# Optimization experiments

Hardware: AMD Instinct MI355X
Metric: run time of the kernel (lower is better)

Reference implementation:

```python
import jax, jax.numpy as jnp
import numpy as np

EPS = 1e-12  # tf.math.l2_normalize epsilon

def _l2norm(v, axis):
    # matches tf.math.l2_normalize: x * rsqrt(max(sum(x^2), eps))
    sq = jnp.sum(v * v, axis=axis, keepdims=True)
    return v * jax.lax.rsqrt(jnp.maximum(sq, EPS))

def setup_inputs() -> dict:
    key = jax.random.key(0)
    ks = jax.random.split(key, 6)
    N, H, W, D, K, OUT = 32, 32, 32, 512, 64, 4096
    x = jax.random.normal(ks[0], (N, H, W, D), dtype=jnp.float32)
    conv1_w = jax.random.normal(ks[1], (D, K), dtype=jnp.float32) * (1.0 / np.sqrt(D))
    conv1_b = jax.random.normal(ks[2], (K,), dtype=jnp.float32) * 0.01
    C = jax.random.uniform(ks[3], (D, K), dtype=jnp.float32)  # tf.random.uniform init
    conv2_w = jax.random.normal(ks[4], (K * D, OUT), dtype=jnp.float32) * (1.0 / np.sqrt(K * D))
    conv2_b = jax.random.normal(ks[5], (OUT,), dtype=jnp.float32) * 0.01
    return {"x": x, "conv1_w": conv1_w, "conv1_b": conv1_b, "C": C,
            "conv2_w": conv2_w, "conv2_b": conv2_b}

def reference(x, conv1_w, conv1_b, C, conv2_w, conv2_b):
    N = x.shape[0]
    # 1x1 conv -> soft assignment over clusters (softmax over last axis)
    s = jax.nn.softmax(jnp.einsum('nhwd,dk->nhwk', x, conv1_w) + conv1_b, axis=-1)  # [N,H,W,K]
    # VLAD: v[n,k,d] = sum_hw s[n,h,w,k] * (x[n,h,w,d] + C[d,k])
    # distributive form avoids the [N,H,W,D,K] intermediate (same math):
    v = jnp.einsum('nhwk,nhwd->nkd', s, x) + jnp.sum(s, axis=(1, 2))[:, :, None] * C.T[None]  # [N,K,D]
    # postnorm: intra-cluster L2 then global-descriptor L2
    v = _l2norm(v, axis=-1)
    v = v.reshape(N, -1)          # flatten [N, K*D]
    v = _l2norm(v, axis=-1)
    # final 1x1 conv (dense projection) + global l2_normalize (tf axis=None)
    v = v @ conv2_w + conv2_b     # [N, 4096]
    v = _l2norm(v, axis=None)     # normalize over the whole tensor (faithful to source)
    return v
```

## Files before the change

### kernel.cpp

```cpp
#include <hip/hip_runtime.h>
#include <math.h>

#define EPSF 1e-12f

typedef __attribute__((ext_vector_type(8))) short short8v;
typedef __attribute__((ext_vector_type(4))) float f32x4;

__device__ __forceinline__ unsigned short f2bf(float f) {
    unsigned int u = __float_as_uint(f);
    return (unsigned short)((u + 0x7FFF + ((u >> 16) & 1)) >> 16);
}
__device__ __forceinline__ float bf2f(unsigned short h) {
    return __uint_as_float(((unsigned int)h) << 16);
}

__global__ __launch_bounds__(256) void k_prep(
    const float* __restrict__ w1, const float* __restrict__ C,
    unsigned short* __restrict__ w1t_h, unsigned short* __restrict__ w1t_l,
    float* __restrict__ Ct)
{
    const int i  = blockIdx.x * 256 + threadIdx.x;
    const int k  = i >> 7;
    const int d0 = (i & 127) << 2;
    float vv[4], cc[4];
#pragma unroll
    for (int j = 0; j < 4; ++j) {
        vv[j] = w1[(size_t)(d0 + j) * 64 + k];
        cc[j] = C [(size_t)(d0 + j) * 64 + k];
    }
    ushort4 h, l;
    h.x = f2bf(vv[0]); l.x = f2bf(vv[0] - bf2f(h.x));
    h.y = f2bf(vv[1]); l.y = f2bf(vv[1] - bf2f(h.y));
    h.z = f2bf(vv[2]); l.z = f2bf(vv[2] - bf2f(h.z));
    h.w = f2bf(vv[3]); l.w = f2bf(vv[3] - bf2f(h.w));
    *(ushort4*)(w1t_h + (size_t)k * 512 + d0) = h;
    *(ushort4*)(w1t_l + (size_t)k * 512 + d0) = l;
    *(float4*)(Ct + (size_t)k * 512 + d0) = make_float4(cc[0], cc[1], cc[2], cc[3]);
}

__global__ __launch_bounds__(256) void k_assign(
    const float* __restrict__ x,
    const unsigned short* __restrict__ w1t_h,
    const unsigned short* __restrict__ w1t_l,
    const float* __restrict__ b1,
    unsigned short* __restrict__ st_h, unsigned short* __restrict__ st_l,
    float* __restrict__ ap)
{
    const int tid  = threadIdx.x;
    const int lane = tid & 63;
    const int wv   = __builtin_amdgcn_readfirstlane(tid >> 6);
    const int l4   = lane >> 4;
    const int l16  = lane & 15;
    const int pix0 = blockIdx.x * 64;
    const int n_img  = blockIdx.x >> 4;
    const int p_base = (blockIdx.x & 15) * 64;

    __shared__ unsigned short Xh[64][72];
    __shared__ unsigned short Xl[64][72];
    __shared__ unsigned short Wh[64][72];
    __shared__ unsigned short Wl[64][72];
    __shared__ float apred[4][64];

    f32x4 acc[4];
#pragma unroll
    for (int nf = 0; nf < 4; ++nf) acc[nf] = (f32x4){0.f, 0.f, 0.f, 0.f};

    float4  xr[4];
    short8v wrh[2], wrl[2];
#pragma unroll
    for (int t = 0; t < 4; ++t) {
        int idx = tid + t * 256, p = idx >> 4, d4 = (idx & 15) << 2;
        xr[t] = *(const float4*)&x[(size_t)(pix0 + p) * 512 + d4];
    }
#pragma unroll
    for (int q = 0; q < 2; ++q) {
        int i = (q * 256 + tid) * 8, k = i >> 6, dd = i & 63;
        wrh[q] = *(const short8v*)(w1t_h + (size_t)k * 512 + dd);
        wrl[q] = *(const short8v*)(w1t_l + (size_t)k * 512 + dd);
    }

    for (int c = 0; c < 8; ++c) {
#pragma unroll
        for (int t = 0; t < 4; ++t) {
            int idx = tid + t * 256, p = idx >> 4, d4 = (idx & 15) << 2;
            float4 v = xr[t];
            ushort4 h4, l4v;
            h4.x = f2bf(v.x); l4v.x = f2bf(v.x - bf2f(h4.x));
            h4.y = f2bf(v.y); l4v.y = f2bf(v.y - bf2f(h4.y));
            h4.z = f2bf(v.z); l4v.z = f2bf(v.z - bf2f(h4.z));
            h4.w = f2bf(v.w); l4v.w = f2bf(v.w - bf2f(h4.w));
            *(ushort4*)&Xh[p][d4] = h4;
            *(ushort4*)&Xl[p][d4] = l4v;
        }
#pragma unroll
        for (int q = 0; q < 2; ++q) {
            int i = (q * 256 + tid) * 8, k = i >> 6, dd = i & 63;
            *(short8v*)&Wh[k][dd] = wrh[q];
            *(short8v*)&Wl[k][dd] = wrl[q];
        }
        if (c + 1 < 8) {
#pragma unroll
            for (int t = 0; t < 4; ++t) {
                int idx = tid + t * 256, p = idx >> 4, d4 = (idx & 15) << 2;
                xr[t] = *(const float4*)&x[(size_t)(pix0 + p) * 512 +
                                           (c + 1) * 64 + d4];
            }
#pragma unroll
            for (int q = 0; q < 2; ++q) {
                int i = (q * 256 + tid) * 8, k = i >> 6, dd = i & 63;
                wrh[q] = *(const short8v*)(w1t_h + (size_t)k * 512 +
                                           (c + 1) * 64 + dd);
                wrl[q] = *(const short8v*)(w1t_l + (size_t)k * 512 +
                                           (c + 1) * 64 + dd);
            }
        }
        __syncthreads();
#pragma unroll
        for (int ks = 0; ks < 2; ++ks) {
            short8v ah = *(const short8v*)&Xh[wv * 16 + l16][ks * 32 + l4 * 8];
            short8v al = *(const short8v*)&Xl[wv * 16 + l16][ks * 32 + l4 * 8];
#pragma unroll
            for (int nf = 0; nf < 4; ++nf) {
                short8v bh = *(const short8v*)&Wh[nf * 16 + l16][ks * 32 + l4 * 8];
                short8v bl = *(const short8v*)&Wl[nf * 16 + l16][ks * 32 + l4 * 8];
                acc[nf] = __builtin_amdgcn_mfma_f32_16x16x32_bf16(ah, bh, acc[nf], 0, 0, 0);
                acc[nf] = __builtin_amdgcn_mfma_f32_16x16x32_bf16(ah, bl, acc[nf], 0, 0, 0);
                acc[nf] = __builtin_amdgcn_mfma_f32_16x16x32_bf16(al, bh, acc[nf], 0, 0, 0);
            }
        }
        __syncthreads();
    }

    float lg[4][4];
#pragma unroll
    for (int nf = 0; nf < 4; ++nf) {
        const float bb = b1[nf * 16 + l16];
#pragma unroll
        for (int r = 0; r < 4; ++r) lg[nf][r] = acc[nf][r] + bb;
    }
    float mx[4], sm[4];
#pragma unroll
    for (int r = 0; r < 4; ++r)
        mx[r] = fmaxf(fmaxf(lg[0][r], lg[1][r]), fmaxf(lg[2][r], lg[3][r]));
#pragma unroll
    for (int m = 1; m <= 8; m <<= 1)
#pragma unroll
        for (int r = 0; r < 4; ++r) mx[r] = fmaxf(mx[r], __shfl_xor(mx[r], m, 64));
#pragma unroll
    for (int r = 0; r < 4; ++r) sm[r] = 0.f;
#pragma unroll
    for (int nf = 0; nf < 4; ++nf)
#pragma unroll
        for (int r = 0; r < 4; ++r) { lg[nf][r] = __expf(lg[nf][r] - mx[r]); sm[r] += lg[nf][r]; }
#pragma unroll
    for (int m = 1; m <= 8; m <<= 1)
#pragma unroll
        for (int r = 0; r < 4; ++r) sm[r] += __shfl_xor(sm[r], m, 64);

#pragma unroll
    for (int nf = 0; nf < 4; ++nf) {
        float sv[4];
        ushort4 hh, ll;
#pragma unroll
        for (int r = 0; r < 4; ++r) sv[r] = lg[nf][r] * (1.0f / sm[r]);
        hh.x = f2bf(sv[0]); ll.x = f2bf(sv[0] - bf2f(hh.x));
        hh.y = f2bf(sv[1]); ll.y = f2bf(sv[1] - bf2f(hh.y));
        hh.z = f2bf(sv[2]); ll.z = f2bf(sv[2] - bf2f(hh.z));
        hh.w = f2bf(sv[3]); ll.w = f2bf(sv[3] - bf2f(hh.w));
        const size_t so = (size_t)(n_img * 64 + nf * 16 + l16) * 1024 +
                          p_base + wv * 16 + l4 * 4;
        *(ushort4*)(st_h + so) = hh;
        *(ushort4*)(st_l + so) = ll;
        float tsum = sv[0] + sv[1] + sv[2] + sv[3];
        tsum += __shfl_xor(tsum, 16, 64);
        tsum += __shfl_xor(tsum, 32, 64);
        if (l4 == 0) apred[wv][nf * 16 + l16] = tsum;
    }
    __syncthreads();
    if (tid < 64)
        ap[(size_t)blockIdx.x * 64 + tid] =
            (apred[0][tid] + apred[1][tid]) + (apred[2][tid] + apred[3][tid]);
}

__global__ __launch_bounds__(128) void k_vlad(
    const unsigned short* __restrict__ st_h,
    const unsigned short* __restrict__ st_l,
    const float* __restrict__ x, float* __restrict__ vpart)
{
    __shared__ float X2[2][32][32];

    const int tid  = threadIdx.x;
    const int lane = tid & 63;
    const int w    = __builtin_amdgcn_readfirstlane(tid >> 6);
    const int l4   = lane >> 4;
    const int l16  = lane & 15;
    const int b    = blockIdx.x;
    const int n    = b >> 5;
    const int ph   = (b >> 4) & 1;
    const int dc   = b & 15;
    const int dbase = dc * 32;
    const int pbase = n * 1024 + ph * 512;

    f32x4 acc[4];
#pragma unroll
    for (int mf = 0; mf < 4; ++mf) acc[mf] = (f32x4){0.f, 0.f, 0.f, 0.f};

#define VSTAGE(T_, B_)                                                        \
    do {                                                                      \
        _Pragma("unroll")                                                     \
        for (int i_ = 0; i_ < 2; ++i_) {                                      \
            const int jj_ = w * 2 + i_;                                       \
            __builtin_amdgcn_global_load_lds(                                 \
                (const __attribute__((address_space(1))) void*)               \
                    (x + (size_t)(pbase + (T_) * 32 + jj_ * 8 +               \
                                  (lane >> 3)) * 512 + dbase + (lane & 7) * 4), \
                (__attribute__((address_space(3))) void*)&X2[B_][jj_ * 8][0], \
                16, 0, 0);                                                    \
        }                                                                     \
    } while (0)

    VSTAGE(0, 0);
    __syncthreads();

    int buf = 0;
    for (int t = 0; t < 16; ++t) {
        if (t + 1 < 16) VSTAGE(t + 1, buf ^ 1);

        const size_t sbase = (size_t)(n * 64) * 1024 + ph * 512 + t * 32 + l4 * 8;
        short8v ah[4], al[4];
#pragma unroll
        for (int mf = 0; mf < 4; ++mf) {
            ah[mf] = *(const short8v*)(st_h + sbase + (size_t)(mf * 16 + l16) * 1024);
            al[mf] = *(const short8v*)(st_l + sbase + (size_t)(mf * 16 + l16) * 1024);
        }
        short8v bh, bl;
#pragma unroll
        for (int j = 0; j < 8; ++j) {
            float bx = X2[buf][l4 * 8 + j][w * 16 + l16];
            unsigned short hb = f2bf(bx);
            bh[j] = (short)hb;
            bl[j] = (short)f2bf(bx - bf2f(hb));
        }
#pragma unroll
        for (int mf = 0; mf < 4; ++mf) {
            acc[mf] = __builtin_amdgcn_mfma_f32_16x16x32_bf16(ah[mf], bh, acc[mf], 0, 0, 0);
            acc[mf] = __builtin_amdgcn_mfma_f32_16x16x32_bf16(ah[mf], bl, acc[mf], 0, 0, 0);
            acc[mf] = __builtin_amdgcn_mfma_f32_16x16x32_bf16(al[mf], bh, acc[mf], 0, 0, 0);
        }
        __syncthreads();
        buf ^= 1;
    }
#undef VSTAGE

#pragma unroll
    for (int mf = 0; mf < 4; ++mf)
#pragma unroll
        for (int r = 0; r < 4; ++r)
            vpart[(size_t)ph * 1048576 +
                  (size_t)(n * 64 + mf * 16 + 4 * l4 + r) * 512 +
                  dbase + w * 16 + l16] = acc[mf][r];
}

__global__ __launch_bounds__(256) void k_norm(
    const float* __restrict__ vpart, const float* __restrict__ ap,
    const float* __restrict__ Ct, unsigned short* __restrict__ vn16)
{
    const int lane = threadIdx.x & 63;
    const int w    = threadIdx.x >> 6;
    const int row  = blockIdx.x * 4 + w;
    const int n    = row >> 6;
    const int k    = row & 63;

    float a_nk = 0.f;
#pragma unroll
    for (int t = 0; t < 16; ++t)
        a_nk += ap[((size_t)(n * 16 + t)) * 64 + k];

    const float* vr0 = vpart + (size_t)row * 512;
    const float* vr1 = vr0 + 1048576;
    const float* cr  = Ct + (size_t)k * 512;
    float vv[8];
    float ss = 0.f;
#pragma unroll
    for (int j = 0; j < 8; ++j) {
        int d = j * 64 + lane;
        float t = (vr0[d] + vr1[d]) + a_nk * cr[d];
        vv[j] = t;
        ss = fmaf(t, t, ss);
    }
#pragma unroll
    for (int off = 32; off > 0; off >>= 1) ss += __shfl_xor(ss, off, 64);
    const float scale = rsqrtf(fmaxf(ss, EPSF)) * 0.125f;
    unsigned short* vo = vn16 + (size_t)row * 512;
#pragma unroll
    for (int j = 0; j < 8; ++j) vo[j * 64 + lane] = f2bf(vv[j] * scale);
}

__global__ __launch_bounds__(256, 2) void k_gemm2(
    const unsigned short* __restrict__ vn16, const float* __restrict__ w2,
    float* __restrict__ outpart)
{
    __shared__ float Bs[3][32][128];

    const int tid  = threadIdx.x;
    const int lane = tid & 63;
    const int wv   = __builtin_amdgcn_readfirstlane(tid >> 6);
    const int kc   = blockIdx.x >> 5;
    const int cb   = blockIdx.x & 31;
    const int rowbase = kc * 2048;
    const int colbase = cb * 128;
    const int l4   = lane >> 4;
    const int l16  = lane & 15;

    f32x4 acc[2][2];
#pragma unroll
    for (int i = 0; i < 2; ++i)
#pragma unroll
        for (int j = 0; j < 2; ++j)
            acc[i][j] = (f32x4){0.f, 0.f, 0.f, 0.f};

#define STAGE(T_, B_)                                                         \
    do {                                                                      \
        _Pragma("unroll")                                                     \
        for (int i_ = 0; i_ < 4; ++i_) {                                      \
            const int r_ = (wv * 4 + i_) * 2 + (lane >> 5);                   \
            __builtin_amdgcn_global_load_lds(                                 \
                (const __attribute__((address_space(1))) void*)               \
                    (w2 + (size_t)(rowbase + (T_) * 32 + r_) * 4096 +         \
                     colbase + (lane & 31) * 4),                              \
                (__attribute__((address_space(3))) void*)                     \
                    &Bs[B_][(wv * 4 + i_) * 2][0],                            \
                16, 0, 0);                                                    \
        }                                                                     \
    } while (0)

    STAGE(0, 0);
    STAGE(1, 1);
    asm volatile("s_waitcnt vmcnt(4)" ::: "memory");
    __builtin_amdgcn_sched_barrier(0);
    __builtin_amdgcn_s_barrier();

    for (int t = 0; t < 64; ++t) {
        const int cur = t % 3;

        const unsigned short* va = vn16 + (size_t)(rowbase + t * 32 + l4 * 8);
        short8v a0 = *(const short8v*)(va + (size_t)l16 * 32768);
        short8v a1 = *(const short8v*)(va + (size_t)(16 + l16) * 32768);

        if (t + 2 < 64) STAGE(t + 2, (t + 2) % 3);

#pragma unroll
        for (int nf = 0; nf < 2; ++nf) {
            const int cl = wv * 32 + nf * 16 + l16;
            short8v bfr;
#pragma unroll
            for (int j = 0; j < 8; ++j)
                bfr[j] = (short)f2bf(Bs[cur][l4 * 8 + j][cl]);
            acc[0][nf] = __builtin_amdgcn_mfma_f32_16x16x32_bf16(
                a0, bfr, acc[0][nf], 0, 0, 0);
            acc[1][nf] = __builtin_amdgcn_mfma_f32_16x16x32_bf16(
                a1, bfr, acc[1][nf], 0, 0, 0);
        }

        if (t + 2 < 64) {
            asm volatile("s_waitcnt vmcnt(4)" ::: "memory");
        } else {
            asm volatile("s_waitcnt vmcnt(0)" ::: "memory");
        }
        __builtin_amdgcn_sched_barrier(0);
        __builtin_amdgcn_s_barrier();
    }
#undef STAGE

#pragma unroll
    for (int mf = 0; mf < 2; ++mf)
#pragma unroll
        for (int nf = 0; nf < 2; ++nf)
#pragma unroll
            for (int r = 0; r < 4; ++r) {
                const int m  = mf * 16 + l4 * 4 + r;
                const int cl = colbase + wv * 32 + nf * 16 + l16;
                outpart[(size_t)kc * 131072 + (size_t)m * 4096 + cl] =
                    acc[mf][nf][r];
            }
}

__global__ __launch_bounds__(256) void k_reduce(
    const float* __restrict__ outpart, const float* __restrict__ b2,
    float* __restrict__ out, float* __restrict__ ssp)
{
    const int i = (blockIdx.x * 256 + threadIdx.x) * 4;
    float4 o = make_float4(0.f, 0.f, 0.f, 0.f);
#pragma unroll
    for (int kc = 0; kc < 16; ++kc) {
        float4 t = *(const float4*)&outpart[(size_t)kc * 131072 + i];
        o.x += t.x; o.y += t.y; o.z += t.z; o.w += t.w;
    }
    float4 bb = *(const float4*)&b2[i & 4095];
    o.x += bb.x; o.y += bb.y; o.z += bb.z; o.w += bb.w;
    *(float4*)&out[i] = o;

    float ss = o.x * o.x + o.y * o.y + o.z * o.z + o.w * o.w;
#pragma unroll
    for (int off = 32; off > 0; off >>= 1) ss += __shfl_xor(ss, off, 64);
    __shared__ float lred[4];
    if ((threadIdx.x & 63) == 0) lred[threadIdx.x >> 6] = ss;
    __syncthreads();
    if (threadIdx.x == 0)
        ssp[blockIdx.x] = lred[0] + lred[1] + lred[2] + lred[3];
}

__global__ __launch_bounds__(256) void k_scale(
    const float* __restrict__ ssp, float* __restrict__ out)
{
    float ss = 0.f;
#pragma unroll
    for (int t = 0; t < 128; ++t) ss += ssp[t];
    const float sc = rsqrtf(fmaxf(ss, EPSF));
    const int i = (blockIdx.x * 256 + threadIdx.x) * 4;
    float4 o = *(float4*)&out[i];
    o.x *= sc; o.y *= sc; o.z *= sc; o.w *= sc;
    *(float4*)&out[i] = o;
}

extern "C" void kernel_launch(void* const* d_in, const int* in_sizes, int n_in,
                              void* d_out, int out_size, void* d_ws, size_t ws_size,
                              hipStream_t stream)
{
    const float* x  = (const float*)d_in[0];
    const float* w1 = (const float*)d_in[1];
    const float* b1 = (const float*)d_in[2];
    const float* C  = (const float*)d_in[3];
    const float* w2 = (const float*)d_in[4];
    const float* b2 = (const float*)d_in[5];
    float* out = (float*)d_out;
    float* ws  = (float*)d_ws;

    unsigned short* st_h  = (unsigned short*)ws;
    unsigned short* st_l  = (unsigned short*)(ws + 1048576);
    float*          vpart = ws + 2097152;
    unsigned short* w1t_h = (unsigned short*)(ws + 4194304);
    unsigned short* w1t_l = (unsigned short*)(ws + 4210688);
    float*          Ct    = ws + 4227072;
    float*          ap    = ws + 4259840;
    float*          ssp   = ws + 4292608;
    unsigned short* vn16  = (unsigned short*)(ws + 4292736);
    float*          outpart = ws + 4817024;

    k_prep  <<<32,   256, 0, stream>>>(w1, C, w1t_h, w1t_l, Ct);
    k_assign<<<512,  256, 0, stream>>>(x, w1t_h, w1t_l, b1, st_h, st_l, ap);
    k_vlad  <<<1024, 128, 0, stream>>>(st_h, st_l, x, vpart);
    k_norm  <<<512,  256, 0, stream>>>(vpart, ap, Ct, vn16);
    k_gemm2 <<<512,  256, 0, stream>>>(vn16, w2, outpart);
    k_reduce<<<128,  256, 0, stream>>>(outpart, b2, out, ssp);
    k_scale <<<128,  256, 0, stream>>>(ssp, out);
}
```

Baseline: 160.3 us.

## Split VLAD pixel range four ways and triple-buffer x staging with vmcnt waits

The k_vlad kernel now splits each image's pixels into four quarters instead of two, doubling the grid to 2048 blocks with eight iterations each. x tiles go through a three-stage LDS ring with explicit vmcnt waits and raw barriers in place of double buffering with __syncthreads. k_norm sums four partial buffers, and the workspace layout is shifted to make room for the larger vpart. The aim is more parallelism and deeper load prefetch, at the cost of extra partial-sum traffic and a more fragile hand-placed wait schedule.

```diff
diff --git a/kernel.cpp b/kernel.cpp
--- a/kernel.cpp
+++ b/kernel.cpp
@@ -187,7 +187,7 @@
     const unsigned short* __restrict__ st_l,
     const float* __restrict__ x, float* __restrict__ vpart)
 {
-    __shared__ float X2[2][32][32];
+    __shared__ float X2[3][32][32];
 
     const int tid  = threadIdx.x;
     const int lane = tid & 63;
@@ -195,11 +195,11 @@
     const int l4   = lane >> 4;
     const int l16  = lane & 15;
     const int b    = blockIdx.x;
-    const int n    = b >> 5;
-    const int ph   = (b >> 4) & 1;
+    const int n    = b >> 6;
+    const int pq   = (b >> 4) & 3;
     const int dc   = b & 15;
     const int dbase = dc * 32;
-    const int pbase = n * 1024 + ph * 512;
+    const int pbase = n * 1024 + pq * 256;
 
     f32x4 acc[4];
 #pragma unroll
@@ -220,23 +220,28 @@
     } while (0)
 
     VSTAGE(0, 0);
-    __syncthreads();
-
-    int buf = 0;
-    for (int t = 0; t < 16; ++t) {
-        if (t + 1 < 16) VSTAGE(t + 1, buf ^ 1);
-
-        const size_t sbase = (size_t)(n * 64) * 1024 + ph * 512 + t * 32 + l4 * 8;
+    VSTAGE(1, 1);
+    asm volatile("s_waitcnt vmcnt(2)" ::: "memory");
+    __builtin_amdgcn_sched_barrier(0);
+    __builtin_amdgcn_s_barrier();
+
+    for (int t = 0; t < 8; ++t) {
+        const int cur = t % 3;
+
+        const size_t sbase = (size_t)(n * 64) * 1024 + pq * 256 + t * 32 + l4 * 8;
         short8v ah[4], al[4];
 #pragma unroll
         for (int mf = 0; mf < 4; ++mf) {
             ah[mf] = *(const short8v*)(st_h + sbase + (size_t)(mf * 16 + l16) * 1024);
             al[mf] = *(const short8v*)(st_l + sbase + (size_t)(mf * 16 + l16) * 1024);
         }
+
+        if (t + 2 < 8) VSTAGE(t + 2, (t + 2) % 3);
+
         short8v bh, bl;
 #pragma unroll
         for (int j = 0; j < 8; ++j) {
-            float bx = X2[buf][l4 * 8 + j][w * 16 + l16];
+            float bx = X2[cur][l4 * 8 + j][w * 16 + l16];
             unsigned short hb = f2bf(bx);
             bh[j] = (short)hb;
             bl[j] = (short)f2bf(bx - bf2f(hb));
@@ -247,8 +252,14 @@
             acc[mf] = __builtin_amdgcn_mfma_f32_16x16x32_bf16(ah[mf], bl, acc[mf], 0, 0, 0);
             acc[mf] = __builtin_amdgcn_mfma_f32_16x16x32_bf16(al[mf], bh, acc[mf], 0, 0, 0);
         }
-        __syncthreads();
-        buf ^= 1;
+
+        if (t + 2 < 8) {
+            asm volatile("s_waitcnt vmcnt(2)" ::: "memory");
+        } else {
+            asm volatile("s_waitcnt vmcnt(0)" ::: "memory");
+        }
+        __builtin_amdgcn_sched_barrier(0);
+        __builtin_amdgcn_s_barrier();
     }
 #undef VSTAGE
 
@@ -256,7 +267,7 @@
     for (int mf = 0; mf < 4; ++mf)
 #pragma unroll
         for (int r = 0; r < 4; ++r)
-            vpart[(size_t)ph * 1048576 +
+            vpart[(size_t)pq * 1048576 +
                   (size_t)(n * 64 + mf * 16 + 4 * l4 + r) * 512 +
                   dbase + w * 16 + l16] = acc[mf][r];
 }
@@ -278,13 +289,15 @@
 
     const float* vr0 = vpart + (size_t)row * 512;
     const float* vr1 = vr0 + 1048576;
+    const float* vr2 = vr0 + 2097152;
+    const float* vr3 = vr0 + 3145728;
     const float* cr  = Ct + (size_t)k * 512;
     float vv[8];
     float ss = 0.f;
 #pragma unroll
     for (int j = 0; j < 8; ++j) {
         int d = j * 64 + lane;
-        float t = (vr0[d] + vr1[d]) + a_nk * cr[d];
+        float t = ((vr0[d] + vr1[d]) + (vr2[d] + vr3[d])) + a_nk * cr[d];
         vv[j] = t;
         ss = fmaf(t, t, ss);
     }
@@ -439,17 +452,17 @@
     unsigned short* st_h  = (unsigned short*)ws;
     unsigned short* st_l  = (unsigned short*)(ws + 1048576);
     float*          vpart = ws + 2097152;
-    unsigned short* w1t_h = (unsigned short*)(ws + 4194304);
-    unsigned short* w1t_l = (unsigned short*)(ws + 4210688);
-    float*          Ct    = ws + 4227072;
-    float*          ap    = ws + 4259840;
-    float*          ssp   = ws + 4292608;
-    unsigned short* vn16  = (unsigned short*)(ws + 4292736);
-    float*          outpart = ws + 4817024;
+    unsigned short* w1t_h = (unsigned short*)(ws + 6291456);
+    unsigned short* w1t_l = (unsigned short*)(ws + 6307840);
+    float*          Ct    = ws + 6324224;
+    float*          ap    = ws + 6356992;
+    float*          ssp   = ws + 6389760;
+    unsigned short* vn16  = (unsigned short*)(ws + 6389888);
+    float*          outpart = ws + 6914176;
 
     k_prep  <<<32,   256, 0, stream>>>(w1, C, w1t_h, w1t_l, Ct);
     k_assign<<<512,  256, 0, stream>>>(x, w1t_h, w1t_l, b1, st_h, st_l, ap);
-    k_vlad  <<<1024, 128, 0, stream>>>(st_h, st_l, x, vpart);
+    k_vlad  <<<2048, 128, 0, stream>>>(st_h, st_l, x, vpart);
     k_norm  <<<512,  256, 0, stream>>>(vpart, ap, Ct, vn16);
     k_gemm2 <<<512,  256, 0, stream>>>(vn16, w2, outpart);
     k_reduce<<<128,  256, 0, stream>>>(outpart, b2, out, ssp);
```

Result: slower. 165.9 us (+3.5%).
